# Kernel optimization log

Hardware: AMD Instinct MI355X
Metric: run time of the kernel (lower is better)

The kernel has to match this reference:

```python
import jax, jax.numpy as jnp
import numpy as np

B, S, D, H, DFF = 2, 2048, 768, 12, 3072
DK = D // H
EPS = 1e-6
NEG = -1e9


def setup_inputs() -> dict:
    key = jax.random.key(0)
    ks = jax.random.split(key, 16)
    s = 1.0 / np.sqrt(D)
    inp = {
        'x': jax.random.normal(ks[0], (B, S, D), jnp.float32),
        'wq': jax.random.normal(ks[1], (D, D), jnp.float32) * s,
        'bq': jnp.zeros((D,), jnp.float32),
        'wk': jax.random.normal(ks[2], (D, D), jnp.float32) * s,
        'bk': jnp.zeros((D,), jnp.float32),
        'wv': jax.random.normal(ks[3], (D, D), jnp.float32) * s,
        'bv': jnp.zeros((D,), jnp.float32),
        'wo': jax.random.normal(ks[4], (D, D), jnp.float32) * s,
        'bo': jnp.zeros((D,), jnp.float32),
        'w1': jax.random.normal(ks[5], (D, DFF), jnp.float32) * s,
        'b1': jnp.zeros((DFF,), jnp.float32),
        'w2': jax.random.normal(ks[6], (DFF, D), jnp.float32) * (1.0 / np.sqrt(DFF)),
        'b2': jnp.zeros((D,), jnp.float32),
        'alpha1': jnp.ones((1,), jnp.float32),
        'beta1': jnp.zeros((1,), jnp.float32),
        'alpha2': jnp.ones((1,), jnp.float32),
        'beta2': jnp.zeros((1,), jnp.float32),
        'mask': jax.random.randint(ks[7], (1, 1, S, S), 0, 2, jnp.int32),
    }
    return inp


def layernorm(x, alpha, beta):
    # torch: mean and UNBIASED std (ddof=1), eps added to std (not variance)
    mean = jnp.mean(x, axis=-1, keepdims=True)
    std = jnp.std(x, axis=-1, keepdims=True, ddof=1)
    return alpha * (x - mean) / (std + EPS) + beta


def encoder_layer(x, wq, bq, wk, bk, wv, bv, wo, bo, w1, b1, w2, b2,
                  alpha1, beta1, alpha2, beta2, mask):
    # projections -> [B, H, S, DK]
    def split_heads(t):
        return t.reshape(B, S, H, DK).transpose(0, 2, 1, 3)
    q = split_heads(x @ wq + bq)
    k = split_heads(x @ wk + bk)
    v = split_heads(x @ wv + bv)
    scores = jnp.einsum('bhqd,bhkd->bhqk', q, k) / np.sqrt(DK)  # [B,H,S,S]
    scores = jnp.where(mask == 0, NEG, scores)
    attn = jax.nn.softmax(scores, axis=-1)
    ctx = jnp.einsum('bhqk,bhkd->bhqd', attn, v)
    ctx = ctx.transpose(0, 2, 1, 3).reshape(B, S, D)
    attn_out = ctx @ wo + bo
    x = layernorm(x + attn_out, alpha1, beta1)
    ff = jax.nn.relu(x @ w1 + b1) @ w2 + b2
    x = layernorm(x + ff, alpha2, beta2)
    return x


def reference(x, wq, bq, wk, bk, wv, bv, wo, bo, w1, b1, w2, b2,
              alpha1, beta1, alpha2, beta2, mask):
    return encoder_layer(x, wq, bq, wk, bk, wv, bv, wo, bo, w1, b1, w2, b2,
                         alpha1, beta1, alpha2, beta2, mask)
```

## Files before the change

### kernel.cpp

```cpp
#include <hip/hip_runtime.h>
#include <hip/hip_bf16.h>


typedef short short8 __attribute__((ext_vector_type(8)));
typedef float floatx4 __attribute__((ext_vector_type(4)));
typedef unsigned short ushort_t;
typedef ushort_t ushort4_t __attribute__((ext_vector_type(4)));

#define B_ 2
#define S_ 2048
#define D_ 768
#define H_ 12
#define DK_ 64
#define DFF_ 3072
#define M_ (B_ * S_)
#define RS_ (3 * D_)

#define LOG2E 1.44269504f
#define FMAX_SHIFT 16.0f

__device__ __forceinline__ float bf2f(ushort_t h) {
  union { unsigned int u; float f; } v; v.u = ((unsigned int)h) << 16; return v.f;
}
__device__ __forceinline__ ushort_t f2bf(float f) {
  union { float f; unsigned int u; } v; v.f = f;
  unsigned int u = v.u;
  unsigned int r = (u + 0x7fffu + ((u >> 16) & 1u)) >> 16;
  return (ushort_t)r;
}

__global__ __launch_bounds__(256) void transpose_f2b(
    const float* __restrict__ in, ushort_t* __restrict__ out, int K, int N) {
  __shared__ ushort_t t[32][33];
  const int nt = blockIdx.x * 32, kt = blockIdx.y * 32;
  const int tx = threadIdx.x, ty = threadIdx.y;
#pragma unroll
  for (int i = 0; i < 4; i++)
    t[ty + i * 8][tx] = f2bf(in[(size_t)(kt + ty + i * 8) * N + nt + tx]);
  __syncthreads();
#pragma unroll
  for (int i = 0; i < 4; i++)
    out[(size_t)(nt + ty + i * 8) * K + kt + tx] = t[tx][ty + i * 8];
}

__global__ __launch_bounds__(256) void transpose4_f2b(
    const float* __restrict__ wq, const float* __restrict__ wk,
    const float* __restrict__ wv, const float* __restrict__ wo,
    ushort_t* __restrict__ wTqkv, ushort_t* __restrict__ woT) {
  __shared__ ushort_t t[32][33];
  const int z = blockIdx.z;
  const float* in = (z == 0) ? wq : (z == 1) ? wk : (z == 2) ? wv : wo;
  ushort_t* out = (z < 3) ? (wTqkv + (size_t)z * D_ * D_) : woT;
  const int nt = blockIdx.x * 32, kt = blockIdx.y * 32;
  const int tx = threadIdx.x, ty = threadIdx.y;
#pragma unroll
  for (int i = 0; i < 4; i++)
    t[ty + i * 8][tx] = f2bf(in[(size_t)(kt + ty + i * 8) * D_ + nt + tx]);
  __syncthreads();
#pragma unroll
  for (int i = 0; i < 4; i++)
    out[(size_t)(nt + ty + i * 8) * D_ + kt + tx] = t[tx][ty + i * 8];
}

__global__ __launch_bounds__(256) void mask_to_biasp(
    const int* __restrict__ mask, ushort_t* __restrict__ out) {
  const int t = blockIdx.x * 256 + threadIdx.x;
  const int q = t >> 8;
  const int cc = t & 255;
  const int k0 = (cc >> 3) * 64;
  const int g = cc & 7, f = g >> 2, lq = g & 3;
  const int* mrow = mask + (size_t)q * S_ + k0;
  const ushort_t cm = f2bf(-1.4427e9f);
  const ushort_t cu = f2bf(-FMAX_SHIFT * LOG2E);
  short8 o;
#pragma unroll
  for (int n2 = 0; n2 < 2; n2++)
#pragma unroll
    for (int r = 0; r < 4; r++) {
      const int kpl = 32 * f + 16 * n2 + 4 * lq + r;
      o[n2 * 4 + r] = (short)((mrow[kpl] == 0) ? cm : cu);
    }
  *(short8*)(out + (size_t)q * S_ + k0 + g * 8) = o;
}

__global__ __launch_bounds__(256) void vtrans(
    const ushort_t* __restrict__ qkv, ushort_t* __restrict__ vt) {
  __shared__ __align__(16) ushort_t T[64 * 72];
  const int tid = threadIdx.x;
  const int bh = blockIdx.y, b = bh / H_, h = bh % H_;
  const int k0 = blockIdx.x * 64;
  const ushort_t* vbase = qkv + (size_t)(b * S_) * RS_ + 2 * D_ + h * DK_;
#pragma unroll
  for (int i = 0; i < 2; i++) {
    const int idx = tid + i * 256;
    const int r = idx >> 3, c = idx & 7;
    short8 vv = *(const short8*)(vbase + (size_t)(k0 + r) * RS_ + c * 8);
    const int sw = (r >> 3) ^ c;
#pragma unroll
    for (int j = 0; j < 8; j++)
      T[(c * 8 + j) * 72 + sw * 8 + (r & 7)] = (ushort_t)vv[j];
  }
  __syncthreads();
#pragma unroll
  for (int i = 0; i < 2; i++) {
    const int ch = tid + i * 256;
    const int d = ch >> 3, g = ch & 7, f = g >> 2, lq = g & 3;
    short8 o;
#pragma unroll
    for (int n2 = 0; n2 < 2; n2++)
#pragma unroll
      for (int r = 0; r < 4; r++) {
        const int kpl = 32 * f + 16 * n2 + 4 * lq + r;
        o[n2 * 4 + r] = (short)T[d * 72 + (((kpl >> 3) ^ (d >> 3)) * 8) + (kpl & 7)];
      }
    *(short8*)(vt + ((size_t)bh * 64 + d) * S_ + k0 + g * 8) = o;
  }
}

__global__ __launch_bounds__(256) void cvt_f2b(
    const float* __restrict__ in, ushort_t* __restrict__ out, int n) {
  const int i = (blockIdx.x * 256 + threadIdx.x) * 4;
  if (i >= n) return;
#pragma unroll
  for (int j = 0; j < 4; j++) out[i + j] = f2bf(in[i + j]);
}

__global__ void concat3(const float* __restrict__ a, const float* __restrict__ b,
                        const float* __restrict__ c, float* __restrict__ o, int n) {
  int i = blockIdx.x * 256 + threadIdx.x;
  if (i >= 3 * n) return;
  o[i] = (i < n) ? a[i] : (i < 2 * n ? b[i - n] : c[i - 2 * n]);
}

template <int BN, bool SPLIT>
__global__ __launch_bounds__(256) void gemm_bt_t(
    const ushort_t* __restrict__ A, const ushort_t* __restrict__ Bt,
    const float* __restrict__ bias, void* __restrict__ Cv,
    int M, int N, int K, int relu, int qcols, float qscale) {
  constexpr int WN = (BN == 128) ? 2 : 1;
  constexpr int WM = 4 / WN;
  constexpr int FI = 128 / WM / 16;
  constexpr int FJ = BN / WN / 16;
  __shared__ __align__(16) ushort_t Al[2][128 * 32];
  __shared__ __align__(16) ushort_t Bl[2][BN * 32];
  const int tid = threadIdx.x;
  const int w = tid >> 6, lane = tid & 63;
  const int wm = (WN == 2) ? (w >> 1) : w;
  const int wn = (WN == 2) ? (w & 1) : 0;
  const int lq = lane >> 4, lr = lane & 15;
  const int m0 = blockIdx.y * 128, n0 = blockIdx.x * BN;

  int kBeg = 0, kEnd = K;
  if (SPLIT) { const int half = K >> 1; kBeg = blockIdx.z * half; kEnd = kBeg + half; }
  const int NT = (kEnd - kBeg) / 32;

  auto stage = [&](int kt, int s) {
    const int k0 = kBeg + kt * 32;
#pragma unroll
    for (int i = 0; i < 2; i++) {
      const int base = (w * 2 + i) * 512;
      const int e = base + lane * 8;
      const int row = e >> 5, col = e & 31;
      __builtin_amdgcn_global_load_lds(
          (const __attribute__((address_space(1))) void*)(A + (size_t)(m0 + row) * K + k0 + col),
          (__attribute__((address_space(3))) void*)(&Al[s][base]), 16, 0, 0);
    }
#pragma unroll
    for (int i = 0; i < BN / 64; i++) {
      const int base = (w * (BN / 64) + i) * 512;
      const int e = base + lane * 8;
      const int row = e >> 5, col = e & 31;
      __builtin_amdgcn_global_load_lds(
          (const __attribute__((address_space(1))) void*)(Bt + (size_t)(n0 + row) * K + k0 + col),
          (__attribute__((address_space(3))) void*)(&Bl[s][base]), 16, 0, 0);
    }
  };

  floatx4 acc[FI][FJ];
#pragma unroll
  for (int i = 0; i < FI; i++)
#pragma unroll
    for (int j = 0; j < FJ; j++) acc[i][j] = (floatx4){0.f, 0.f, 0.f, 0.f};

  stage(0, 0);
  for (int kt = 0; kt < NT; kt++) {
    const int s = kt & 1;
    __syncthreads();
    if (kt + 1 < NT) stage(kt + 1, s ^ 1);

    short8 af[FI], bf[FJ];
#pragma unroll
    for (int i = 0; i < FI; i++)
      af[i] = *(const short8*)&Al[s][(wm * (FI * 16) + i * 16 + lr) * 32 + lq * 8];
#pragma unroll
    for (int j = 0; j < FJ; j++)
      bf[j] = *(const short8*)&Bl[s][(wn * (FJ * 16) + j * 16 + lr) * 32 + lq * 8];
#pragma unroll
    for (int i = 0; i < FI; i++)
#pragma unroll
      for (int j = 0; j < FJ; j++)
        acc[i][j] = __builtin_amdgcn_mfma_f32_16x16x32_bf16(af[i], bf[j], acc[i][j], 0, 0, 0);
  }

#pragma unroll
  for (int i = 0; i < FI; i++) {
    const int m = m0 + wm * (FI * 16) + i * 16 + lq * 4;
#pragma unroll
    for (int j = 0; j < FJ; j++) {
      const int n = n0 + wn * (FJ * 16) + j * 16 + lr;
      if (SPLIT) {
        float* P = (float*)Cv + (size_t)blockIdx.z * M * N;
#pragma unroll
        for (int r = 0; r < 4; r++)
          P[(size_t)(m + r) * N + n] = acc[i][j][r];
      } else {
        const float bv = bias[n];
#pragma unroll
        for (int r = 0; r < 4; r++) {
          float v = acc[i][j][r] + bv;
          if (n < qcols) v *= qscale;
          if (relu) v = v > 0.f ? v : 0.f;
          ((ushort_t*)Cv)[(size_t)(m + r) * N + n] = f2bf(v);
        }
      }
    }
  }
}

__global__ __launch_bounds__(256, 3) void flash_attn(
    const ushort_t* __restrict__ qkv, const ushort_t* __restrict__ vt,
    const ushort_t* __restrict__ maskp, ushort_t* __restrict__ ctx) {
  __shared__ __align__(16) ushort_t lds[2][3][64 * 64];
  const int tid = threadIdx.x;
  const int w = tid >> 6, lane = tid & 63;
  const int lq = lane >> 4, lr = lane & 15;
  const int blk = blockIdx.x;
  const int bh = blk >> 5, qb = blk & 31;
  const int b = bh / H_, h = bh % H_;
  const int q0 = qb * 64;
  const ushort_t* qbase = qkv + (size_t)(b * S_) * RS_ + h * DK_;
  const ushort_t* kbase = qbase + D_;
  const ushort_t* vtb   = vt + (size_t)bh * DK_ * S_;
  const ushort_t* mb    = maskp + (size_t)q0 * S_;

  short8 qfr[2];
#pragma unroll
  for (int f = 0; f < 2; f++)
    qfr[f] = *(const short8*)(
        qbase + (size_t)(q0 + w * 16 + lr) * RS_ + f * 32 + lq * 8);

  auto stage = [&](int k0, int s) {
#pragma unroll
    for (int i = 0; i < 2; i++) {
      const int id = i * 256 + tid;
      const int row = id >> 3;
      const int cc = ((id & 7) ^ (row & 7)) * 8;
      const int dbase = (i * 256 + w * 64) * 8;
      __builtin_amdgcn_global_load_lds(
          (const __attribute__((address_space(1))) void*)(kbase + (size_t)(k0 + row) * RS_ + cc),
          (__attribute__((address_space(3))) void*)(&lds[s][0][dbase]), 16, 0, 0);
      __builtin_amdgcn_global_load_lds(
          (const __attribute__((address_space(1))) void*)(vtb + (size_t)row * S_ + k0 + cc),
          (__attribute__((address_space(3))) void*)(&lds[s][1][dbase]), 16, 0, 0);
      __builtin_amdgcn_global_load_lds(
          (const __attribute__((address_space(1))) void*)(mb + (size_t)row * S_ + k0 + cc),
          (__attribute__((address_space(3))) void*)(&lds[s][2][dbase]), 16, 0, 0);
    }
  };

  floatx4 oacc[4];
#pragma unroll
  for (int dt = 0; dt < 4; dt++) oacc[dt] = (floatx4){0.f, 0.f, 0.f, 0.f};
  float li = 0.f;

  stage(0, 0);
  __syncthreads();

  const int sw8 = lr & 7;
  const int c0 = (lq ^ sw8) * 8;
  const int c1 = ((4 + lq) ^ sw8) * 8;

  for (int t = 0; t < S_ / 64; t++) {
    const int s = t & 1;
    stage((t + 1) * 64, s ^ 1);

    const ushort_t* kl = &lds[s][0][0];
    const ushort_t* vl = &lds[s][1][0];
    const ushort_t* ml = &lds[s][2][0];

    const int mrow = (w * 16 + lr) * 64;
    short8 bb0 = *(const short8*)(ml + mrow + c0);
    short8 bb1 = *(const short8*)(ml + mrow + c1);

    floatx4 sacc[4];
#pragma unroll
    for (int n = 0; n < 4; n++) sacc[n] = (floatx4){0.f, 0.f, 0.f, 0.f};
#pragma unroll
    for (int n = 0; n < 4; n++) {
      const int krow = (n * 16 + lr) * 64;
      short8 a0 = *(const short8*)(kl + krow + c0);
      short8 a1 = *(const short8*)(kl + krow + c1);
      sacc[n] = __builtin_amdgcn_mfma_f32_16x16x32_bf16(a0, qfr[0], sacc[n], 0, 0, 0);
      sacc[n] = __builtin_amdgcn_mfma_f32_16x16x32_bf16(a1, qfr[1], sacc[n], 0, 0, 0);
    }

    short8 pf[2];
#pragma unroll
    for (int f = 0; f < 2; f++) {
      const short8 bb = f ? bb1 : bb0;
      union { __hip_bfloat162 h2[4]; short8 v; } u;
#pragma unroll
      for (int jj = 0; jj < 4; jj++) {
        const int e0 = jj * 2, e1 = jj * 2 + 1;
        float2 p2;
        p2.x = __builtin_amdgcn_exp2f(sacc[2 * f + (e0 >> 2)][e0 & 3] + bf2f((ushort_t)bb[e0]));
        p2.y = __builtin_amdgcn_exp2f(sacc[2 * f + (e1 >> 2)][e1 & 3] + bf2f((ushort_t)bb[e1]));
        li += p2.x + p2.y;
        u.h2[jj] = __float22bfloat162_rn(p2);
      }
      pf[f] = u.v;
    }

#pragma unroll
    for (int dt = 0; dt < 4; dt++) {
      const int vrow = (dt * 16 + lr) * 64;
      short8 v0 = *(const short8*)(vl + vrow + c0);
      short8 v1 = *(const short8*)(vl + vrow + c1);
      oacc[dt] = __builtin_amdgcn_mfma_f32_16x16x32_bf16(v0, pf[0], oacc[dt], 0, 0, 0);
      oacc[dt] = __builtin_amdgcn_mfma_f32_16x16x32_bf16(v1, pf[1], oacc[dt], 0, 0, 0);
    }
    __syncthreads();
  }

  li += __shfl_xor(li, 16);
  li += __shfl_xor(li, 32);
  const float inv = 1.f / (li + 1e-37f);

  const size_t row = (size_t)(b * S_ + q0 + w * 16 + lr) * D_ + h * DK_;
#pragma unroll
  for (int dt = 0; dt < 4; dt++) {
    ushort4_t o;
#pragma unroll
    for (int r = 0; r < 4; r++) o[r] = f2bf(oacc[dt][r] * inv);
    *(ushort4_t*)(ctx + row + dt * 16 + lq * 4) = o;
  }
}

template <bool XF, bool OF>
__global__ __launch_bounds__(256) void add_ln_comb(
    const void* __restrict__ xv, const float* __restrict__ P0,
    const float* __restrict__ P1, const float* __restrict__ cb,
    const float* __restrict__ alpha, const float* __restrict__ beta,
    void* __restrict__ outv) {
  const int row = blockIdx.x, tid = threadIdx.x;
  const int w = tid >> 6, lane = tid & 63;
  __shared__ float red[8];
  float v[3];
#pragma unroll
  for (int i = 0; i < 3; i++) {
    const int c = tid + i * 256;
    const size_t idx = (size_t)row * D_ + c;
    float xv_;
    if (XF) xv_ = ((const float*)xv)[idx];
    else    xv_ = bf2f(((const ushort_t*)xv)[idx]);
    v[i] = xv_ + (P0[idx] + P1[idx] + cb[c]);
  }
  float s = v[0] + v[1] + v[2];
#pragma unroll
  for (int off = 1; off < 64; off <<= 1) s += __shfl_xor(s, off);
  if (lane == 0) red[w] = s;
  __syncthreads();
  const float mean = (red[0] + red[1] + red[2] + red[3]) / (float)D_;
  float d = 0.f;
#pragma unroll
  for (int i = 0; i < 3; i++) { const float t = v[i] - mean; d += t * t; }
#pragma unroll
  for (int off = 1; off < 64; off <<= 1) d += __shfl_xor(d, off);
  if (lane == 0) red[4 + w] = d;
  __syncthreads();
  const float var = (red[4] + red[5] + red[6] + red[7]) / (float)(D_ - 1);
  const float inv = 1.f / (sqrtf(var) + 1e-6f);
  const float a = alpha[0] * inv, bt = beta[0];
#pragma unroll
  for (int i = 0; i < 3; i++) {
    const int c = tid + i * 256;
    const float o = a * (v[i] - mean) + bt;
    if (OF) ((float*)outv)[(size_t)row * D_ + c] = o;
    else    ((ushort_t*)outv)[(size_t)row * D_ + c] = f2bf(o);
  }
}

extern "C" void kernel_launch(void* const* d_in, const int* in_sizes, int n_in,
                              void* d_out, int out_size, void* d_ws, size_t ws_size,
                              hipStream_t stream) {
  const float* x   = (const float*)d_in[0];
  const float* wq  = (const float*)d_in[1];
  const float* bq  = (const float*)d_in[2];
  const float* wk  = (const float*)d_in[3];
  const float* bk  = (const float*)d_in[4];
  const float* wv  = (const float*)d_in[5];
  const float* bv  = (const float*)d_in[6];
  const float* wo  = (const float*)d_in[7];
  const float* bo  = (const float*)d_in[8];
  const float* w1  = (const float*)d_in[9];
  const float* b1  = (const float*)d_in[10];
  const float* w2  = (const float*)d_in[11];
  const float* b2  = (const float*)d_in[12];
  const float* a1  = (const float*)d_in[13];
  const float* be1 = (const float*)d_in[14];
  const float* a2  = (const float*)d_in[15];
  const float* be2 = (const float*)d_in[16];
  const int*   msk = (const int*)d_in[17];

  const size_t E_xb    = 0;
  const size_t E_wTqkv = E_xb    + (size_t)M_ * D_;
  const size_t E_woT   = E_wTqkv + (size_t)3 * D_ * D_;
  const size_t E_w1T   = E_woT   + (size_t)D_ * D_;
  const size_t E_w2T   = E_w1T   + (size_t)DFF_ * D_;
  const size_t E_bqkv  = E_w2T   + (size_t)D_ * DFF_;
  const size_t E_qkv   = E_bqkv  + (size_t)2 * 3 * D_;
  const size_t E_ctx   = E_qkv   + (size_t)M_ * 3 * D_;
  const size_t E_attn  = E_ctx   + (size_t)M_ * D_;
  const size_t E_x1    = E_attn  + (size_t)M_ * D_;
  const size_t E_h1    = E_x1    + (size_t)M_ * D_;
  const size_t E_ff    = E_h1    + (size_t)M_ * DFF_;
  const size_t E_total = E_ff    + (size_t)M_ * D_;
  if (ws_size < E_total * sizeof(ushort_t)) return;

  ushort_t* ws    = (ushort_t*)d_ws;
  ushort_t* xb    = ws + E_xb;
  ushort_t* wTqkv = ws + E_wTqkv;
  ushort_t* woT   = ws + E_woT;
  ushort_t* w1T   = ws + E_w1T;
  ushort_t* w2T   = ws + E_w2T;
  float*    bqkv  = (float*)(ws + E_bqkv);
  ushort_t* qkv   = ws + E_qkv;
  ushort_t* ctx   = ws + E_ctx;
  ushort_t* x1    = ws + E_x1;
  ushort_t* h1    = ws + E_h1;
  ushort_t* maskp = ws + E_h1;
  ushort_t* vt    = ws + E_h1 + (size_t)S_ * S_;
  float*    Pattn = (float*)(ws + E_h1);
  float*    Pff2  = (float*)(ws + E_qkv);

  const float SCALE_Q = 0.125f * LOG2E;

  const dim3 tb(32, 8);
  transpose4_f2b<<<dim3(24, 24, 4), tb, 0, stream>>>(wq, wk, wv, wo, wTqkv, woT);
  transpose_f2b<<<dim3(96, 24), tb, 0, stream>>>(w1, w1T, D_, DFF_);
  transpose_f2b<<<dim3(24, 96), tb, 0, stream>>>(w2, w2T, DFF_, D_);
  mask_to_biasp<<<(S_ * S_ / 8) / 256, 256, 0, stream>>>(msk, maskp);
  concat3<<<9, 256, 0, stream>>>(bq, bk, bv, bqkv, D_);
  cvt_f2b<<<(M_ * D_ / 4 + 255) / 256, 256, 0, stream>>>(x, xb, M_ * D_);

  gemm_bt_t<64, false><<<dim3(36, 32), 256, 0, stream>>>(
      xb, wTqkv, bqkv, qkv, M_, 3 * D_, D_, 0, D_, SCALE_Q);
  vtrans<<<dim3(S_ / 64, B_ * H_), 256, 0, stream>>>(qkv, vt);
  flash_attn<<<(B_ * H_) * (S_ / 64), 256, 0, stream>>>(qkv, vt, maskp, ctx);
  gemm_bt_t<64, true><<<dim3(12, 32, 2), 256, 0, stream>>>(
      ctx, woT, nullptr, Pattn, M_, D_, D_, 0, 0, 1.f);
  add_ln_comb<true, false><<<M_, 256, 0, stream>>>(
      x, Pattn, Pattn + (size_t)M_ * D_, bo, a1, be1, x1);
  gemm_bt_t<128, false><<<dim3(24, 32), 256, 0, stream>>>(
      x1, w1T, b1, h1, M_, DFF_, D_, 1, 0, 1.f);
  gemm_bt_t<64, true><<<dim3(12, 32, 2), 256, 0, stream>>>(
      h1, w2T, nullptr, Pff2, M_, D_, DFF_, 0, 0, 1.f);
  add_ln_comb<false, true><<<M_, 256, 0, stream>>>(
      x1, Pff2, Pff2 + (size_t)M_ * D_, b2, a2, be2, d_out);
}
```

Before: 309.9 us.

## Swizzle GEMM blocks per XCD, store split-K partials as bf16, reorder attention blocks

GEMM launches become 1D grids whose block index is remapped so that each of the 8 XCDs owns a contiguous range of M tiles, aiming for better L2 reuse of A rows. The split-K partial sums are written as bf16 instead of fp32, halving partial-buffer traffic into the add+LayerNorm kernels, at some cost in precision. Flash-attention block ordering is switched to interleave heads across consecutive blocks, which spreads K/V reads across XCDs.

```diff
diff --git a/kernel.cpp b/kernel.cpp
--- a/kernel.cpp
+++ b/kernel.cpp
@@ -141,6 +141,7 @@
   constexpr int WM = 4 / WN;
   constexpr int FI = 128 / WM / 16;
   constexpr int FJ = BN / WN / 16;
+  constexpr int Z = SPLIT ? 2 : 1;
   __shared__ __align__(16) ushort_t Al[2][128 * 32];
   __shared__ __align__(16) ushort_t Bl[2][BN * 32];
   const int tid = threadIdx.x;
@@ -148,10 +149,19 @@
   const int wm = (WN == 2) ? (w >> 1) : w;
   const int wn = (WN == 2) ? (w & 1) : 0;
   const int lq = lane >> 4, lr = lane & 15;
-  const int m0 = blockIdx.y * 128, n0 = blockIdx.x * BN;
+
+  const int NT_n = N / BN;
+  const int mg = M >> 10;
+  const int lin = blockIdx.x;
+  const int xcd = lin & 7, idx = lin >> 3;
+  const int m_t = xcd * mg + idx / (NT_n * Z);
+  const int rem = idx % (NT_n * Z);
+  const int n_t = rem % NT_n;
+  const int z   = rem / NT_n;
+  const int m0 = m_t * 128, n0 = n_t * BN;
 
   int kBeg = 0, kEnd = K;
-  if (SPLIT) { const int half = K >> 1; kBeg = blockIdx.z * half; kEnd = kBeg + half; }
+  if (SPLIT) { const int half = K >> 1; kBeg = z * half; kEnd = kBeg + half; }
   const int NT = (kEnd - kBeg) / 32;
 
   auto stage = [&](int kt, int s) {
@@ -209,10 +219,10 @@
     for (int j = 0; j < FJ; j++) {
       const int n = n0 + wn * (FJ * 16) + j * 16 + lr;
       if (SPLIT) {
-        float* P = (float*)Cv + (size_t)blockIdx.z * M * N;
+        ushort_t* P = (ushort_t*)Cv + (size_t)z * M * N;
 #pragma unroll
         for (int r = 0; r < 4; r++)
-          P[(size_t)(m + r) * N + n] = acc[i][j][r];
+          P[(size_t)(m + r) * N + n] = f2bf(acc[i][j][r]);
       } else {
         const float bv = bias[n];
 #pragma unroll
@@ -235,7 +245,7 @@
   const int w = tid >> 6, lane = tid & 63;
   const int lq = lane >> 4, lr = lane & 15;
   const int blk = blockIdx.x;
-  const int bh = blk >> 5, qb = blk & 31;
+  const int bh = blk % (B_ * H_), qb = blk / (B_ * H_);
   const int b = bh / H_, h = bh % H_;
   const int q0 = qb * 64;
   const ushort_t* qbase = qkv + (size_t)(b * S_) * RS_ + h * DK_;
@@ -348,8 +358,8 @@
 
 template <bool XF, bool OF>
 __global__ __launch_bounds__(256) void add_ln_comb(
-    const void* __restrict__ xv, const float* __restrict__ P0,
-    const float* __restrict__ P1, const float* __restrict__ cb,
+    const void* __restrict__ xv, const ushort_t* __restrict__ P0,
+    const ushort_t* __restrict__ P1, const float* __restrict__ cb,
     const float* __restrict__ alpha, const float* __restrict__ beta,
     void* __restrict__ outv) {
   const int row = blockIdx.x, tid = threadIdx.x;
@@ -363,7 +373,7 @@
     float xv_;
     if (XF) xv_ = ((const float*)xv)[idx];
     else    xv_ = bf2f(((const ushort_t*)xv)[idx]);
-    v[i] = xv_ + (P0[idx] + P1[idx] + cb[c]);
+    v[i] = xv_ + (bf2f(P0[idx]) + bf2f(P1[idx]) + cb[c]);
   }
   float s = v[0] + v[1] + v[2];
 #pragma unroll
@@ -440,8 +450,8 @@
   ushort_t* h1    = ws + E_h1;
   ushort_t* maskp = ws + E_h1;
   ushort_t* vt    = ws + E_h1 + (size_t)S_ * S_;
-  float*    Pattn = (float*)(ws + E_h1);
-  float*    Pff2  = (float*)(ws + E_qkv);
+  ushort_t* Pattn = ws + E_h1;
+  ushort_t* Pff2  = ws + E_qkv;
 
   const float SCALE_Q = 0.125f * LOG2E;
 
@@ -453,17 +463,17 @@
   concat3<<<9, 256, 0, stream>>>(bq, bk, bv, bqkv, D_);
   cvt_f2b<<<(M_ * D_ / 4 + 255) / 256, 256, 0, stream>>>(x, xb, M_ * D_);
 
-  gemm_bt_t<64, false><<<dim3(36, 32), 256, 0, stream>>>(
+  gemm_bt_t<64, false><<<1152, 256, 0, stream>>>(
       xb, wTqkv, bqkv, qkv, M_, 3 * D_, D_, 0, D_, SCALE_Q);
   vtrans<<<dim3(S_ / 64, B_ * H_), 256, 0, stream>>>(qkv, vt);
   flash_attn<<<(B_ * H_) * (S_ / 64), 256, 0, stream>>>(qkv, vt, maskp, ctx);
-  gemm_bt_t<64, true><<<dim3(12, 32, 2), 256, 0, stream>>>(
+  gemm_bt_t<64, true><<<768, 256, 0, stream>>>(
       ctx, woT, nullptr, Pattn, M_, D_, D_, 0, 0, 1.f);
   add_ln_comb<true, false><<<M_, 256, 0, stream>>>(
       x, Pattn, Pattn + (size_t)M_ * D_, bo, a1, be1, x1);
-  gemm_bt_t<128, false><<<dim3(24, 32), 256, 0, stream>>>(
+  gemm_bt_t<128, false><<<768, 256, 0, stream>>>(
       x1, w1T, b1, h1, M_, DFF_, D_, 1, 0, 1.f);
-  gemm_bt_t<64, true><<<dim3(12, 32, 2), 256, 0, stream>>>(
+  gemm_bt_t<64, true><<<768, 256, 0, stream>>>(
       h1, w2T, nullptr, Pff2, M_, D_, DFF_, 0, 0, 1.f);
   add_ln_comb<false, true><<<M_, 256, 0, stream>>>(
       x1, Pff2, Pff2 + (size_t)M_ * D_, b2, a2, be2, d_out);
```

New measurement: 303.5 us. -2.1%, faster.
